# Kernel tuning notes

Measured on AMD Instinct MI355X. Metric: run time of the kernel, lower is better.

The kernel has to match this reference:

```python
import jax, jax.numpy as jnp
import numpy as np

THITA = 0.0001

def conv1x1_relu(x, w, b):
    # x: [B,C_in,H,W], w: [C_out,C_in], b: [C_out]; 1x1 conv + bias + ReLU
    return jax.nn.relu(jnp.einsum('bchw,oc->bohw', x, w) + b[None, :, None, None])

def down4(x):
    # F.interpolate(x, scale_factor=0.25), mode='nearest': input idx = floor(i/0.25) = 4*i
    return x[:, :, ::4, ::4]

def up4(x):
    return jnp.repeat(jnp.repeat(x, 4, axis=2), 4, axis=3)

def setup_inputs() -> dict:
    key = jax.random.key(0)
    ks = jax.random.split(key, 16)
    B, C, H, W = 4, 64, 256, 256
    s = 1.0 / np.sqrt(C)
    inp = {
        'x1': jax.random.normal(ks[0], (B, 2 * C, H, W), jnp.float32),
        'x2': jax.random.normal(ks[1], (B, C, H, W), jnp.float32),
        'event': jax.random.normal(ks[2], (B, C, H, W), jnp.float32),
        # x_feature_extract: 3C->C then C->C
        'xw0': jax.random.normal(ks[3], (C, 3 * C), jnp.float32) * (1.0 / np.sqrt(3 * C)),
        'xb0': jax.random.normal(ks[4], (C,), jnp.float32) * 0.01,
        'xw1': jax.random.normal(ks[5], (C, C), jnp.float32) * s,
        'xb1': jax.random.normal(ks[6], (C,), jnp.float32) * 0.01,
        # event_feature_extract: C->C then C->C
        'ew0': jax.random.normal(ks[7], (C, C), jnp.float32) * s,
        'eb0': jax.random.normal(ks[8], (C,), jnp.float32) * 0.01,
        'ew1': jax.random.normal(ks[9], (C, C), jnp.float32) * s,
        'eb1': jax.random.normal(ks[10], (C,), jnp.float32) * 0.01,
        # query / key / value 1x1 convs
        'qw': jax.random.normal(ks[11], (C, C), jnp.float32) * s,
        'qb': jnp.zeros((C,), jnp.float32),
        'kw': jax.random.normal(ks[12], (C, C), jnp.float32) * s,
        'kb': jnp.zeros((C,), jnp.float32),
        'vw': jax.random.normal(ks[13], (C, C), jnp.float32) * s,
        'vb': jnp.zeros((C,), jnp.float32),
        'gamma': jax.random.normal(ks[14], (1,), jnp.float32),
    }
    return inp

def reference(x1, x2, event, xw0, xb0, xw1, xb1, ew0, eb0, ew1, eb1, qw, qb, kw, kb, vw, vb, gamma):
    x = jnp.concatenate([x1, x2], axis=1)                 # [B,3C,H,W]
    x = conv1x1_relu(x, xw0, xb0)                         # [B,C,H,W]
    ef = conv1x1_relu(event, ew0, eb0)                    # [B,C,H,W]
    x_2 = down4(x)                                        # [B,C,H/4,W/4]
    ef = down4(ef)
    x_2 = conv1x1_relu(x_2, xw1, xb1)
    ef = conv1x1_relu(ef, ew1, eb1)
    B, C, h, w = x_2.shape
    N = h * w
    q = conv1x1_relu(x_2, qw, qb).reshape(B, C, N)        # [B,C,N]
    k = conv1x1_relu(ef, kw, kb).reshape(B, C, N)         # [B,C,N]
    energy = jnp.einsum('bcn,bcm->bnm', q, k)             # [B,N,N]
    attention = jax.nn.softmax(energy, axis=-1)
    v = conv1x1_relu(x_2, vw, vb).reshape(B, C, N)        # [B,C,N]
    out = jnp.einsum('bcn,bmn->bcm', v, attention)        # bmm(v, att^T)
    out = out.reshape(B, C, h, w)
    out = up4(out)                                        # [B,C,H,W]
    out = gamma * out
    out = THITA * out + x
    ef_up = up4(ef)
    return (out, ef_up)
```

## Files before the change

### kernel.cpp

```cpp
#include <hip/hip_runtime.h>

typedef __attribute__((ext_vector_type(8))) short bf16x8;
typedef __attribute__((ext_vector_type(4))) float f32x4;

__device__ __forceinline__ unsigned pk2(float f0, float f1) {
  return __builtin_amdgcn_perm(__float_as_uint(f1) + 0x8000u,
                               __float_as_uint(f0) + 0x8000u, 0x07060302u);
}
__device__ __forceinline__ short f2bf_s(float f) {
  return (short)((__float_as_uint(f) + 0x8000u) >> 16);
}
__device__ __forceinline__ float bf2f(short s) {
  return __uint_as_float(((unsigned)(unsigned short)s) << 16);
}

__global__ __launch_bounds__(256, 3) void k1_conv192(
    const float* __restrict__ x1, const float* __restrict__ x2,
    const float* __restrict__ w0, const float* __restrict__ b0,
    float* __restrict__ xout, short* __restrict__ xds)
{
  const int b    = blockIdx.y;
  const int wv   = threadIdx.x >> 6;
  const int lane = threadIdx.x & 63;
  const int quad = lane >> 4;
  const int l16  = lane & 15;
  const int n0   = blockIdx.x * 256 + wv * 64;

  f32x4 acc[4][4];
  #pragma unroll
  for (int mt = 0; mt < 4; ++mt)
    #pragma unroll
    for (int nt = 0; nt < 4; ++nt)
      acc[mt][nt] = (f32x4){0.f, 0.f, 0.f, 0.f};

  #pragma unroll
  for (int kc = 0; kc < 6; ++kc) {
    bf16x8 af[4];
    #pragma unroll
    for (int mt = 0; mt < 4; ++mt) {
      const float* wrow = w0 + (mt * 16 + l16) * 192 + kc * 32 + quad * 8;
      float4 wa = *(const float4*)wrow;
      float4 wb = *(const float4*)(wrow + 4);
      union { unsigned i[4]; bf16x8 v; } u;
      u.i[0] = pk2(wa.x, wa.y); u.i[1] = pk2(wa.z, wa.w);
      u.i[2] = pk2(wb.x, wb.y); u.i[3] = pk2(wb.z, wb.w);
      af[mt] = u.v;
    }
    const float* src = (kc < 4)
        ? (x1 + ((long)b * 128 + kc * 32) * 65536)
        : (x2 + ((long)b * 64 + (kc - 4) * 32) * 65536);
    const float* s8 = src + (long)(quad * 8) * 65536;
    bf16x8 bfv[4];
    #pragma unroll
    for (int nt = 0; nt < 4; ++nt) {
      const int p = n0 + nt * 16 + l16;
      float e[8];
      #pragma unroll
      for (int j = 0; j < 8; ++j) e[j] = s8[(long)j * 65536 + p];
      union { unsigned i[4]; bf16x8 v; } u;
      #pragma unroll
      for (int j = 0; j < 4; ++j) u.i[j] = pk2(e[2 * j], e[2 * j + 1]);
      bfv[nt] = u.v;
    }
    #pragma unroll
    for (int mt = 0; mt < 4; ++mt)
      #pragma unroll
      for (int nt = 0; nt < 4; ++nt)
        acc[mt][nt] = __builtin_amdgcn_mfma_f32_16x16x32_bf16(
            af[mt], bfv[nt], acc[mt][nt], 0, 0, 0);
  }

  #pragma unroll
  for (int mt = 0; mt < 4; ++mt) {
    const float4 bb = *(const float4*)(b0 + mt * 16 + quad * 4);
    #pragma unroll
    for (int r = 0; r < 4; ++r) {
      const int o = mt * 16 + quad * 4 + r;
      const float bias = (r == 0) ? bb.x : (r == 1) ? bb.y : (r == 2) ? bb.z : bb.w;
      float* orow = xout + ((long)b * 64 + o) * 65536;
      #pragma unroll
      for (int nt = 0; nt < 4; ++nt)
        orow[n0 + nt * 16 + l16] = fmaxf(acc[mt][nt][r] + bias, 0.f);
    }
  }
  if (((blockIdx.x & 3) == 0) && ((l16 & 3) == 0)) {
    const int nbase = (blockIdx.x >> 2) * 64 + wv * 16 + (l16 >> 2);
    #pragma unroll
    for (int mt = 0; mt < 4; ++mt) {
      const float4 bb = *(const float4*)(b0 + mt * 16 + quad * 4);
      #pragma unroll
      for (int nt = 0; nt < 4; ++nt) {
        const float v0 = fmaxf(acc[mt][nt][0] + bb.x, 0.f);
        const float v1 = fmaxf(acc[mt][nt][1] + bb.y, 0.f);
        const float v2 = fmaxf(acc[mt][nt][2] + bb.z, 0.f);
        const float v3 = fmaxf(acc[mt][nt][3] + bb.w, 0.f);
        union { unsigned i[2]; unsigned long long q; } u;
        u.i[0] = pk2(v0, v1); u.i[1] = pk2(v2, v3);
        const int n = nbase + nt * 4;
        *(unsigned long long*)(xds + ((long)b * 4096 + n) * 64 + mt * 16 + quad * 4) = u.q;
      }
    }
  }
}

__device__ __forceinline__ void loadw_frag(const float* __restrict__ w,
                                           int row, int quad, bf16x8 wf[2]) {
  #pragma unroll
  for (int kc = 0; kc < 2; ++kc) {
    const float* p = w + row * 64 + kc * 32 + quad * 8;
    float4 a = *(const float4*)p;
    float4 c = *(const float4*)(p + 4);
    union { unsigned i[4]; bf16x8 v; } u;
    u.i[0] = pk2(a.x, a.y); u.i[1] = pk2(a.z, a.w);
    u.i[2] = pk2(c.x, c.y); u.i[3] = pk2(c.z, c.w);
    wf[kc] = u.v;
  }
}

__device__ __forceinline__ void conv_mfma(const short (*src)[72], short (*dst)[72],
                                          const bf16x8* wf,
                                          const float* __restrict__ bias,
                                          int ch0, int l16, int quad) {
  const float4 bv4 = *(const float4*)(bias + ch0);
  #pragma unroll
  for (int nt = 0; nt < 4; ++nt) {
    f32x4 acc = (f32x4){0.f, 0.f, 0.f, 0.f};
    #pragma unroll
    for (int kc = 0; kc < 2; ++kc) {
      bf16x8 bv = *(const bf16x8*)&src[nt * 16 + l16][kc * 32 + quad * 8];
      acc = __builtin_amdgcn_mfma_f32_16x16x32_bf16(wf[kc], bv, acc, 0, 0, 0);
    }
    const float v0 = fmaxf(acc[0] + bv4.x, 0.f);
    const float v1 = fmaxf(acc[1] + bv4.y, 0.f);
    const float v2 = fmaxf(acc[2] + bv4.z, 0.f);
    const float v3 = fmaxf(acc[3] + bv4.w, 0.f);
    union { unsigned i[2]; unsigned long long q; } u;
    u.i[0] = pk2(v0, v1); u.i[1] = pk2(v2, v3);
    *(unsigned long long*)&dst[nt * 16 + l16][ch0] = u.q;
  }
}

__global__ __launch_bounds__(256) void k2_small(
    const short* __restrict__ xds, const float* __restrict__ event,
    const float* __restrict__ xw1, const float* __restrict__ xb1,
    const float* __restrict__ ew0, const float* __restrict__ eb0,
    const float* __restrict__ ew1, const float* __restrict__ eb1,
    const float* __restrict__ qw, const float* __restrict__ qb,
    const float* __restrict__ kw, const float* __restrict__ kb,
    const float* __restrict__ vw, const float* __restrict__ vb,
    short* __restrict__ q_pm, short* __restrict__ k_pm,
    short* __restrict__ v_cm, short* __restrict__ ef_cm)
{
  __shared__ short A[64][72], Bb[64][72], Cb[64][72];
  const int b    = blockIdx.y;
  const int h4   = blockIdx.x;
  const int t    = threadIdx.x;
  const int lane = t & 63;
  const int g    = t >> 6;
  const int quad = lane >> 4;
  const int l16  = lane & 15;
  const int row  = g * 16 + l16;
  const int ch0  = g * 16 + quad * 4;

  bf16x8 wfx1[2], wfq[2], wfv[2], wfe0[2], wfe1[2], wfk[2];
  loadw_frag(xw1, row, quad, wfx1);
  loadw_frag(qw,  row, quad, wfq);
  loadw_frag(vw,  row, quad, wfv);
  loadw_frag(ew0, row, quad, wfe0);
  loadw_frag(ew1, row, quad, wfe1);
  loadw_frag(kw,  row, quad, wfk);

  const int px  = t >> 2;
  const int seg = t & 3;
  {
    const short* s = xds + ((long)b * 4096 + h4 * 64 + px) * 64 + seg * 16;
    *(bf16x8*)&A[px][seg * 16]     = *(const bf16x8*)s;
    *(bf16x8*)&A[px][seg * 16 + 8] = *(const bf16x8*)(s + 8);
  }
  __syncthreads();
  conv_mfma(A, Bb, wfx1, xb1, ch0, l16, quad);
  __syncthreads();
  conv_mfma(Bb, A,  wfq, qb, ch0, l16, quad);
  conv_mfma(Bb, Cb, wfv, vb, ch0, l16, quad);
  __syncthreads();
  {
    short* qdst = q_pm + ((long)b * 4096 + h4 * 64 + px) * 64 + seg * 16;
    *(bf16x8*)qdst       = *(const bf16x8*)&A[px][seg * 16];
    *(bf16x8*)(qdst + 8) = *(const bf16x8*)&A[px][seg * 16 + 8];
    union { short s[16]; int4 q2[2]; } vv;
    #pragma unroll
    for (int i = 0; i < 16; ++i) vv.s[i] = Cb[seg * 16 + i][px];
    int4* vdst = (int4*)(v_cm + ((long)b * 64 + px) * 4096 + h4 * 64 + seg * 16);
    vdst[0] = vv.q2[0]; vdst[1] = vv.q2[1];
    const int px2 = t & 63, cg = t >> 6;
    const float* ev = event + (long)b * 64 * 65536 + (long)h4 * 1024 + px2 * 4;
    #pragma unroll
    for (int r = 0; r < 16; r += 2) {
      const float e0v = ev[(long)(cg * 16 + r) * 65536];
      const float e1v = ev[(long)(cg * 16 + r + 1) * 65536];
      *(unsigned*)&Bb[px2][cg * 16 + r] = pk2(e0v, e1v);
    }
  }
  __syncthreads();
  conv_mfma(Bb, A,  wfe0, eb0, ch0, l16, quad);
  __syncthreads();
  conv_mfma(A,  Cb, wfe1, eb1, ch0, l16, quad);
  __syncthreads();
  conv_mfma(Cb, Bb, wfk, kb, ch0, l16, quad);
  {
    union { short s[16]; int4 q2[2]; } vv;
    #pragma unroll
    for (int i = 0; i < 16; ++i) vv.s[i] = Cb[seg * 16 + i][px];
    int4* edst = (int4*)(ef_cm + ((long)b * 64 + px) * 4096 + h4 * 64 + seg * 16);
    edst[0] = vv.q2[0]; edst[1] = vv.q2[1];
  }
  __syncthreads();
  {
    short* kdst = k_pm + ((long)b * 4096 + h4 * 64 + px) * 64 + seg * 16;
    *(bf16x8*)kdst       = *(const bf16x8*)&Bb[px][seg * 16];
    *(bf16x8*)(kdst + 8) = *(const bf16x8*)&Bb[px][seg * 16 + 8];
  }
}

__global__ __launch_bounds__(256, 4) void k3_attn(
    const short* __restrict__ q_pm, const short* __restrict__ k_pm,
    const short* __restrict__ v_cm, short* __restrict__ Opart,
    float* __restrict__ ml)
{
  __shared__ short Kf[2][4096];
  __shared__ short Vf[2][4096];
  __shared__ short Pf[4][2][512];
  const int b    = blockIdx.y;
  const int ks   = blockIdx.z;
  const int q0   = blockIdx.x * 64;
  const int t    = threadIdx.x;
  const int wv   = __builtin_amdgcn_readfirstlane(t >> 6);
  const int lane = t & 63;
  const int quad = lane >> 4;
  const int l16  = lane & 15;

  bf16x8 qf[2];
  {
    const short* qp = q_pm + ((long)b * 4096 + q0 + wv * 16 + l16) * 64 + quad * 8;
    qf[0] = *(const bf16x8*)qp;
    qf[1] = *(const bf16x8*)(qp + 32);
  }

  const int srow  = t >> 2;
  const int seg   = t & 3;
  const int doff0 = (((seg >> 1) * 4 + (srow >> 4)) * 64 +
                     ((seg & 1) * 2) * 16 + (srow & 15)) * 8;
  const short* kbase = k_pm + (long)b * 4096 * 64;
  const short* vbase = v_cm + (long)b * 64 * 4096;
  const int kt0 = ks * 16;

  bf16x8 krg[2], vrg[2];
  {
    const short* s = kbase + (long)(kt0 * 64 + srow) * 64 + seg * 16;
    krg[0] = *(const bf16x8*)s; krg[1] = *(const bf16x8*)(s + 8);
    const short* v = vbase + (long)srow * 4096 + kt0 * 64 + seg * 16;
    vrg[0] = *(const bf16x8*)v; vrg[1] = *(const bf16x8*)(v + 8);
  }
  *(bf16x8*)&Kf[0][doff0]       = krg[0];
  *(bf16x8*)&Kf[0][doff0 + 128] = krg[1];
  *(bf16x8*)&Vf[0][doff0]       = vrg[0];
  *(bf16x8*)&Vf[0][doff0 + 128] = vrg[1];
  __syncthreads();

  f32x4 oacc[4];
  #pragma unroll
  for (int f = 0; f < 4; ++f) oacc[f] = (f32x4){0, 0, 0, 0};
  float run_m = -1e30f, run_l = 0.f;

  for (int kt = 0; kt < 16; ++kt) {
    if (kt < 15) {
      const int k0 = (kt0 + kt + 1) * 64;
      const short* s = kbase + (long)(k0 + srow) * 64 + seg * 16;
      krg[0] = *(const bf16x8*)s; krg[1] = *(const bf16x8*)(s + 8);
      const short* v = vbase + (long)srow * 4096 + k0 + seg * 16;
      vrg[0] = *(const bf16x8*)v; vrg[1] = *(const bf16x8*)(v + 8);
    }
    const int buf = kt & 1;

    f32x4 st[4];
    #pragma unroll
    for (int f = 0; f < 4; ++f) st[f] = (f32x4){0, 0, 0, 0};
    #pragma unroll
    for (int kc = 0; kc < 2; ++kc)
      #pragma unroll
      for (int f = 0; f < 4; ++f) {
        bf16x8 ka = *(const bf16x8*)&Kf[buf][((kc * 4 + f) * 64 + lane) * 8];
        st[f] = __builtin_amdgcn_mfma_f32_16x16x32_bf16(ka, qf[kc], st[f], 0, 0, 0);
      }

    float tm = st[0][0];
    #pragma unroll
    for (int f = 0; f < 4; ++f)
      #pragma unroll
      for (int r = 0; r < 4; ++r) tm = fmaxf(tm, st[f][r]);
    tm = fmaxf(tm, __shfl_xor(tm, 16));
    tm = fmaxf(tm, __shfl_xor(tm, 32));
    const float nm = fmaxf(run_m, tm);
    const float al = __expf(run_m - nm);
    run_m = nm;
    float pf[4][4], ts = 0.f;
    #pragma unroll
    for (int f = 0; f < 4; ++f)
      #pragma unroll
      for (int r = 0; r < 4; ++r) {
        pf[f][r] = __expf(st[f][r] - nm);
        ts += pf[f][r];
      }
    ts += __shfl_xor(ts, 16);
    ts += __shfl_xor(ts, 32);
    run_l = run_l * al + ts;
    #pragma unroll
    for (int f = 0; f < 4; ++f)
      #pragma unroll
      for (int r = 0; r < 4; ++r) oacc[f][r] *= al;

    #pragma unroll
    for (int f = 0; f < 4; ++f) {
      union { unsigned i[2]; unsigned long long q; } u;
      u.i[0] = pk2(pf[f][0], pf[f][1]);
      u.i[1] = pk2(pf[f][2], pf[f][3]);
      const int qd = (f & 1) * 2 + (quad >> 1);
      *(unsigned long long*)&Pf[wv][f >> 1][(qd * 16 + l16) * 8 + (quad & 1) * 4] = u.q;
    }
    #pragma unroll
    for (int kc = 0; kc < 2; ++kc) {
      bf16x8 pb = *(const bf16x8*)&Pf[wv][kc][lane * 8];
      #pragma unroll
      for (int f = 0; f < 4; ++f) {
        bf16x8 va = *(const bf16x8*)&Vf[buf][((kc * 4 + f) * 64 + lane) * 8];
        oacc[f] = __builtin_amdgcn_mfma_f32_16x16x32_bf16(va, pb, oacc[f], 0, 0, 0);
      }
    }

    if (kt < 15) {
      const int nb = buf ^ 1;
      *(bf16x8*)&Kf[nb][doff0]       = krg[0];
      *(bf16x8*)&Kf[nb][doff0 + 128] = krg[1];
      *(bf16x8*)&Vf[nb][doff0]       = vrg[0];
      *(bf16x8*)&Vf[nb][doff0 + 128] = vrg[1];
      __syncthreads();
    }
  }

  const int q = q0 + wv * 16 + l16;
  #pragma unroll
  for (int f = 0; f < 4; ++f)
    #pragma unroll
    for (int r = 0; r < 4; ++r) {
      const int ch = f * 16 + quad * 4 + r;
      Opart[((long)(ks * 4 + b) * 64 + ch) * 4096 + q] = f2bf_s(oacc[f][r]);
    }
  if (quad == 0) {
    float2 v = make_float2(run_m, run_l);
    *(float2*)&ml[((long)(ks * 4 + b) * 4096 + q) * 2] = v;
  }
}

__global__ __launch_bounds__(256) void k3w(const float* __restrict__ ml,
                                           float* __restrict__ wc)
{
  const int idx = blockIdx.x * 256 + threadIdx.x;
  const float2* m2 = (const float2*)ml;
  float2 s0 = m2[0 * 16384 + idx];
  float2 s1 = m2[1 * 16384 + idx];
  float2 s2 = m2[2 * 16384 + idx];
  float2 s3 = m2[3 * 16384 + idx];
  const float M = fmaxf(fmaxf(s0.x, s1.x), fmaxf(s2.x, s3.x));
  const float e0 = __expf(s0.x - M), e1 = __expf(s1.x - M);
  const float e2 = __expf(s2.x - M), e3 = __expf(s3.x - M);
  const float inv = 1.f / (e0 * s0.y + e1 * s1.y + e2 * s2.y + e3 * s3.y);
  *(float4*)&wc[idx * 4] = make_float4(e0 * inv, e1 * inv, e2 * inv, e3 * inv);
}

__global__ __launch_bounds__(256) void k4_final(
    const short* __restrict__ Opart, const float* __restrict__ wc,
    const short* __restrict__ ef_cm, const float* __restrict__ gamma,
    float* __restrict__ dout)
{
  const long idx = (long)blockIdx.x * 256 + threadIdx.x;
  const long e4 = idx * 4;
  const int hw = (int)(e4 & 65535);
  const int bc = (int)(e4 >> 16);
  const int h = hw >> 8, w0 = hw & 255;
  const int n = (h >> 2) * 64 + (w0 >> 2);
  const int b = bc >> 6, c = bc & 63;
  const float s = 1e-4f * gamma[0];
  const float4 w4 = *(const float4*)&wc[((long)b * 4096 + n) * 4];
  const long obase = ((long)b * 64 + c) * 4096 + n;
  float ov = w4.x * bf2f(Opart[obase]) +
             w4.y * bf2f(Opart[obase + (long)1 * 4 * 64 * 4096]) +
             w4.z * bf2f(Opart[obase + (long)2 * 4 * 64 * 4096]) +
             w4.w * bf2f(Opart[obase + (long)3 * 4 * 64 * 4096]);
  ov *= s;
  float4 xv = *(float4*)(dout + e4);
  xv.x += ov; xv.y += ov; xv.z += ov; xv.w += ov;
  *(float4*)(dout + e4) = xv;
  const float ef = bf2f(ef_cm[(long)bc * 4096 + n]);
  *(float4*)(dout + 16777216 + e4) = make_float4(ef, ef, ef, ef);
}

extern "C" void kernel_launch(void* const* d_in, const int* in_sizes, int n_in,
                              void* d_out, int out_size, void* d_ws, size_t ws_size,
                              hipStream_t stream)
{
  const float* x1    = (const float*)d_in[0];
  const float* x2    = (const float*)d_in[1];
  const float* event = (const float*)d_in[2];
  const float* xw0   = (const float*)d_in[3];
  const float* xb0   = (const float*)d_in[4];
  const float* xw1   = (const float*)d_in[5];
  const float* xb1   = (const float*)d_in[6];
  const float* ew0   = (const float*)d_in[7];
  const float* eb0   = (const float*)d_in[8];
  const float* ew1   = (const float*)d_in[9];
  const float* eb1   = (const float*)d_in[10];
  const float* qw    = (const float*)d_in[11];
  const float* qb    = (const float*)d_in[12];
  const float* kw    = (const float*)d_in[13];
  const float* kb    = (const float*)d_in[14];
  const float* vw    = (const float*)d_in[15];
  const float* vb    = (const float*)d_in[16];
  const float* gamma = (const float*)d_in[17];
  float* dout = (float*)d_out;

  char* ws = (char*)d_ws;
  short* q_pm  = (short*)(ws);
  short* k_pm  = (short*)(ws + (2u << 20));
  short* v_cm  = (short*)(ws + (4u << 20));
  short* ef_cm = (short*)(ws + (6u << 20));
  short* xds   = (short*)(ws + (8u << 20));
  short* Opart = (short*)(ws + (10u << 20));
  float* ml    = (float*)(ws + (18u << 20));
  float* wc    = (float*)(ws + (18u << 20) + (512u << 10));

  k1_conv192<<<dim3(256, 4), 256, 0, stream>>>(x1, x2, xw0, xb0, dout, xds);
  k2_small<<<dim3(64, 4), 256, 0, stream>>>(xds, event, xw1, xb1, ew0, eb0,
                                            ew1, eb1, qw, qb, kw, kb, vw, vb,
                                            q_pm, k_pm, v_cm, ef_cm);
  k3_attn<<<dim3(64, 4, 4), 256, 0, stream>>>(q_pm, k_pm, v_cm, Opart, ml);
  k3w<<<64, 256, 0, stream>>>(ml, wc);
  k4_final<<<16384, 256, 0, stream>>>(Opart, wc, ef_cm, gamma, dout);
}
```

Before: 419.4 us.

## Double-buffer conv192 input tiles in LDS via async global_load_lds

```diff
diff --git a/kernel.cpp b/kernel.cpp
--- a/kernel.cpp
+++ b/kernel.cpp
@@ -14,28 +14,33 @@
   return __uint_as_float(((unsigned)(unsigned short)s) << 16);
 }
 
-__global__ __launch_bounds__(256, 3) void k1_conv192(
+__device__ __forceinline__ void gload16(const float* gp, float* lp) {
+  __builtin_amdgcn_global_load_lds(
+      reinterpret_cast<const __attribute__((address_space(1))) void*>(
+          reinterpret_cast<unsigned long long>(gp)),
+      reinterpret_cast<__attribute__((address_space(3))) void*>(
+          (unsigned)reinterpret_cast<unsigned long long>(lp)),
+      16, 0, 0);
+}
+
+__global__ __launch_bounds__(256, 2) void k1_conv192(
     const float* __restrict__ x1, const float* __restrict__ x2,
     const float* __restrict__ w0, const float* __restrict__ b0,
     float* __restrict__ xout, short* __restrict__ xds)
 {
+  __shared__ float X[2][32][256];
   const int b    = blockIdx.y;
-  const int wv   = threadIdx.x >> 6;
-  const int lane = threadIdx.x & 63;
+  const int t    = threadIdx.x;
+  const int wv   = t >> 6;
+  const int lane = t & 63;
   const int quad = lane >> 4;
   const int l16  = lane & 15;
-  const int n0   = blockIdx.x * 256 + wv * 64;
-
-  f32x4 acc[4][4];
-  #pragma unroll
-  for (int mt = 0; mt < 4; ++mt)
-    #pragma unroll
-    for (int nt = 0; nt < 4; ++nt)
-      acc[mt][nt] = (f32x4){0.f, 0.f, 0.f, 0.f};
-
-  #pragma unroll
-  for (int kc = 0; kc < 6; ++kc) {
-    bf16x8 af[4];
+  const int n0   = blockIdx.x * 256;
+  const int nw   = n0 + wv * 64;
+
+  bf16x8 af[6][4];
+  #pragma unroll
+  for (int kc = 0; kc < 6; ++kc)
     #pragma unroll
     for (int mt = 0; mt < 4; ++mt) {
       const float* wrow = w0 + (mt * 16 + l16) * 192 + kc * 32 + quad * 8;
@@ -44,22 +49,52 @@
       union { unsigned i[4]; bf16x8 v; } u;
       u.i[0] = pk2(wa.x, wa.y); u.i[1] = pk2(wa.z, wa.w);
       u.i[2] = pk2(wb.x, wb.y); u.i[3] = pk2(wb.z, wb.w);
-      af[mt] = u.v;
-    }
-    const float* src = (kc < 4)
-        ? (x1 + ((long)b * 128 + kc * 32) * 65536)
-        : (x2 + ((long)b * 64 + (kc - 4) * 32) * 65536);
-    const float* s8 = src + (long)(quad * 8) * 65536;
+      af[kc][mt] = u.v;
+    }
+
+  f32x4 acc[4][4];
+  #pragma unroll
+  for (int mt = 0; mt < 4; ++mt)
+    #pragma unroll
+    for (int nt = 0; nt < 4; ++nt)
+      acc[mt][nt] = (f32x4){0.f, 0.f, 0.f, 0.f};
+
+  const int pg = 4 * (lane ^ ((wv & 1) << 2));
+  auto stage = [&](int kc, int buf) {
+    const float* src = (kc < 4) ? (x1 + ((long)b * 128 + kc * 32) * 65536)
+                                : (x2 + ((long)b * 64 + (kc - 4) * 32) * 65536);
+    #pragma unroll
+    for (int i = 0; i < 8; ++i) {
+      const int c = wv * 8 + i;
+      gload16(src + (long)c * 65536 + n0 + pg, &X[buf][c][0]);
+    }
+  };
+
+  stage(0, 0);
+  #pragma unroll
+  for (int kc = 0; kc < 6; ++kc) {
+    if (kc < 5) {
+      stage(kc + 1, (kc + 1) & 1);
+      asm volatile("s_waitcnt vmcnt(8)" ::: "memory");
+    } else {
+      asm volatile("s_waitcnt vmcnt(0)" ::: "memory");
+    }
+    __builtin_amdgcn_s_barrier();
+    asm volatile("" ::: "memory");
+
     bf16x8 bfv[4];
     #pragma unroll
     for (int nt = 0; nt < 4; ++nt) {
-      const int p = n0 + nt * 16 + l16;
-      float e[8];
-      #pragma unroll
-      for (int j = 0; j < 8; ++j) e[j] = s8[(long)j * 65536 + p];
+      const int Gg = wv * 16 + nt * 4 + (l16 >> 2);
       union { unsigned i[4]; bf16x8 v; } u;
       #pragma unroll
-      for (int j = 0; j < 4; ++j) u.i[j] = pk2(e[2 * j], e[2 * j + 1]);
+      for (int jp = 0; jp < 4; ++jp) {
+        const int c0  = quad * 8 + 2 * jp;
+        const int idx = ((Gg ^ ((quad & 1) << 2)) << 2) | (l16 & 3);
+        const float e0 = X[kc & 1][c0][idx];
+        const float e1 = X[kc & 1][c0 + 1][idx];
+        u.i[jp] = pk2(e0, e1);
+      }
       bfv[nt] = u.v;
     }
     #pragma unroll
@@ -67,7 +102,13 @@
       #pragma unroll
       for (int nt = 0; nt < 4; ++nt)
         acc[mt][nt] = __builtin_amdgcn_mfma_f32_16x16x32_bf16(
-            af[mt], bfv[nt], acc[mt][nt], 0, 0, 0);
+            af[kc][mt], bfv[nt], acc[mt][nt], 0, 0, 0);
+
+    if (kc < 5) {
+      asm volatile("s_waitcnt lgkmcnt(0)" ::: "memory");
+      __builtin_amdgcn_s_barrier();
+      asm volatile("" ::: "memory");
+    }
   }
 
   #pragma unroll
@@ -80,7 +121,7 @@
       float* orow = xout + ((long)b * 64 + o) * 65536;
       #pragma unroll
       for (int nt = 0; nt < 4; ++nt)
-        orow[n0 + nt * 16 + l16] = fmaxf(acc[mt][nt][r] + bias, 0.f);
+        orow[nw + nt * 16 + l16] = fmaxf(acc[mt][nt][r] + bias, 0.f);
     }
   }
   if (((blockIdx.x & 3) == 0) && ((l16 & 3) == 0)) {
```

Result: slower. 431.4 us (+2.9%).
